# Optimization experiments

Measured on AMD Instinct MI355X. Metric: run time of the kernel, lower is better.

## Reference

```python
import jax, jax.numpy as jnp
import numpy as np

B, T, N, D = 16, 12, 325, 1
K, H = 3, 64
ST, Z, LH = 95, 32, 128
MI = ST + Z  # 127


def _mlp(x, w1, b1, w2, b2):
    return jnp.maximum(x @ w1 + b1, 0.0) @ w2 + b2


def setup_inputs() -> dict:
    key = jax.random.key(0)
    ks = jax.random.split(key, 20)
    inp = {
        "G": jax.random.normal(ks[0], (K, N, N), jnp.float32) * (1.0 / np.sqrt(N)),
        "x": jax.random.normal(ks[1], (B, T, N, D), jnp.float32),
        "meta_input": jax.random.normal(ks[2], (B, N, MI), jnp.float32),
    }
    s = 0.02
    outs = {"lwg": K * (D + H) * 2 * H, "lbg": 2 * H, "lwu": K * (D + H) * H, "lbu": H}
    i = 3
    for name, od in outs.items():
        inp[name + "_w1"] = jax.random.normal(ks[i], (MI, LH), jnp.float32) * s; i += 1
        inp[name + "_b1"] = jnp.zeros((LH,), jnp.float32)
        inp[name + "_w2"] = jax.random.normal(ks[i], (LH, od), jnp.float32) * s; i += 1
        inp[name + "_b2"] = jnp.zeros((od,), jnp.float32)
    return inp


def reference(G, x, meta_input,
              lwg_w1, lwg_b1, lwg_w2, lwg_b2,
              lbg_w1, lbg_b1, lbg_w2, lbg_b2,
              lwu_w1, lwu_b1, lwu_w2, lwu_b2,
              lbu_w1, lbu_b1, lbu_w2, lbu_b2):
    # hypernetwork: per-(batch, node) GCN weights
    Wg = _mlp(meta_input, lwg_w1, lwg_b1, lwg_w2, lwg_b2).reshape(B, N, K * (D + H), 2 * H)
    bg = _mlp(meta_input, lbg_w1, lbg_b1, lbg_w2, lbg_b2)          # [B,N,2H]
    Wu = _mlp(meta_input, lwu_w1, lwu_b1, lwu_w2, lwu_b2).reshape(B, N, K * (D + H), H)
    bu = _mlp(meta_input, lbu_w1, lbu_b1, lbu_w2, lbu_b2)          # [B,N,H]

    def gcn(inp, W, b):
        # Chebyshev hops stacked along k (matches torch.cat over k-blocks)
        sup = jnp.einsum('knm,bmi->bnki', G, inp)                  # [B,N,K,i]
        sup = sup.reshape(B, N, -1)                                # [B,N,K*i]
        return jnp.einsum('bni,bnih->bnh', sup, W) + b

    def step(h, xt):
        comb = jnp.concatenate([xt, h], axis=-1)                   # [B,N,D+H]
        zr = jax.nn.sigmoid(gcn(comb, Wg, bg))
        z, r = zr[..., :H], zr[..., H:]
        cand = jnp.concatenate([xt, r * h], axis=-1)
        n = jnp.tanh(gcn(cand, Wu, bu))
        h = z * n + (1.0 - z) * h
        return h, h

    h0 = jnp.zeros((B, N, H), x.dtype)
    h_last, hs = jax.lax.scan(step, h0, jnp.moveaxis(x, 1, 0))     # hs: [T,B,N,H]
    return jnp.moveaxis(hs, 0, 1), h_last
```

## Files before the change

kernel.cpp:

```cpp
#include <hip/hip_runtime.h>
#include <hip/hip_bf16.h>
#include <stdint.h>

#define Bc   16
#define Tc   12
#define Nc   325
#define Kc   3
#define Hc   64
#define MIc  127
#define LHc  128
#define BNc  (Bc*Nc)
#define SUPW 195
#define NCg  (SUPW*2*Hc)
#define NCu  (SUPW*Hc)
#define MP   163
#define MCH  6

typedef _Float16 half8  __attribute__((ext_vector_type(8)));
typedef _Float16 half2v __attribute__((ext_vector_type(2)));
typedef float    f32x4  __attribute__((ext_vector_type(4)));

static __device__ __forceinline__ float bflo(unsigned int u) {
    return __uint_as_float(u << 16);
}
static __device__ __forceinline__ float bfhi(unsigned int u) {
    return __uint_as_float(u & 0xffff0000u);
}
static __device__ __forceinline__ unsigned short f2bf(float f) {
    unsigned int u = __float_as_uint(f);
    unsigned int r = (u + 0x7fffu + ((u >> 16) & 1u)) >> 16;
    return (unsigned short)r;
}
static __device__ __forceinline__ float fdot2f(half2v a, half2v b, float c) {
#if defined(__has_builtin)
#if __has_builtin(__builtin_amdgcn_fdot2)
    return __builtin_amdgcn_fdot2(a, b, c, false);
#else
    return c + (float)a[0] * (float)b[0] + (float)a[1] * (float)b[1];
#endif
#else
    return c + (float)a[0] * (float)b[0] + (float)a[1] * (float)b[1];
#endif
}
static __device__ __forceinline__ unsigned int packh2(float a, float b) {
    half2v h; h[0] = (_Float16)a; h[1] = (_Float16)b;
    return *(unsigned int*)&h;
}

__global__ __launch_bounds__(128) void meta1_kernel(
    const float* __restrict__ meta,
    const float* __restrict__ w1a, const float* __restrict__ b1a,
    const float* __restrict__ w1b, const float* __restrict__ b1b,
    const float* __restrict__ w1c, const float* __restrict__ b1c,
    const float* __restrict__ w1d, const float* __restrict__ b1d,
    _Float16* __restrict__ r1a, _Float16* __restrict__ r1b,
    _Float16* __restrict__ r1c, _Float16* __restrict__ r1d)
{
    __shared__ float mrow[4][128];
    const int bn0 = blockIdx.x * 4;
    const int l   = threadIdx.x;
#pragma unroll
    for (int r = 0; r < 4; r++)
        mrow[r][l] = (l < MIc) ? meta[(size_t)(bn0 + r) * MIc + l] : 0.f;
    __syncthreads();

    const float* w1s[4] = {w1a, w1b, w1c, w1d};
    const float* b1s[4] = {b1a, b1b, b1c, b1d};
    _Float16*    os[4]  = {r1a, r1b, r1c, r1d};
#pragma unroll
    for (int s = 0; s < 4; s++) {
        const float* w = w1s[s];
        float acc[4];
        const float bv = b1s[s][l];
#pragma unroll
        for (int r = 0; r < 4; r++) acc[r] = bv;
        for (int m = 0; m < MIc; m++) {
            float wv = w[m * LHc + l];
#pragma unroll
            for (int r = 0; r < 4; r++) acc[r] = fmaf(mrow[r][m], wv, acc[r]);
        }
#pragma unroll
        for (int r = 0; r < 4; r++)
            os[s][(size_t)(bn0 + r) * LHc + l] = (_Float16)fmaxf(acc[r], 0.f);
    }
}

__global__ __launch_bounds__(256) void transpose_w2_kernel(
    const float* __restrict__ w2, _Float16* __restrict__ w2t, int NC)
{
    __shared__ float Ls[128][65];
    const int c0 = blockIdx.x * 64;
    const int t  = threadIdx.x;
    {
        const int c  = t & 63;
        const int kb = t >> 6;
        for (int k = kb; k < 128; k += 4) {
            int cc = c0 + c;
            Ls[k][c] = (cc < NC) ? w2[(size_t)k * NC + cc] : 0.f;
        }
    }
    __syncthreads();
    {
        const int k  = t & 127;
        const int ch = t >> 7;
        for (int c = ch; c < 64; c += 2) {
            int cc = c0 + c;
            if (cc < NC) w2t[(size_t)cc * 128 + k] = (_Float16)Ls[k][c];
        }
    }
}

template<bool BF16OUT>
__global__ __launch_bounds__(256) void meta2_mfma_kernel(
    const _Float16* __restrict__ A,
    const _Float16* __restrict__ Bt,
    const float* __restrict__ bias,
    void* __restrict__ outp, int NC, int nrows)
{
    __shared__ __align__(16) _Float16 As[64][136];
    __shared__ __align__(16) _Float16 Bs[64][136];
    __shared__ unsigned short Cs[64][72];
    const int t  = threadIdx.x;
    const int w  = t >> 6;
    const int l  = t & 63;
    const int r0 = blockIdx.x * 64;
    const int c0 = blockIdx.y * 64;

#pragma unroll
    for (int p = 0; p < 4; p++) {
        const int gid = p * 256 + t;
        const int row = gid >> 4;
        const int cg  = gid & 15;
        half8 av = (half8)(_Float16)0.f;
        if (r0 + row < nrows) av = *(const half8*)(A + (size_t)(r0 + row) * 128 + cg * 8);
        *(half8*)&As[row][cg * 8] = av;
        half8 bv = *(const half8*)(Bt + (size_t)(c0 + row) * 128 + cg * 8);
        *(half8*)&Bs[row][cg * 8] = bv;
    }
    __syncthreads();

    const int lr = l & 15;
    const int lk = l >> 4;

    half8 aF[4];
#pragma unroll
    for (int kk = 0; kk < 4; kk++)
        aF[kk] = *(const half8*)&As[w * 16 + lr][kk * 32 + lk * 8];

    f32x4 acc[4];
#pragma unroll
    for (int j = 0; j < 4; j++) acc[j] = (f32x4)0.f;

#pragma unroll
    for (int j = 0; j < 4; j++)
#pragma unroll
        for (int kk = 0; kk < 4; kk++) {
            half8 bF = *(const half8*)&Bs[j * 16 + lr][kk * 32 + lk * 8];
            acc[j] = __builtin_amdgcn_mfma_f32_16x16x32_f16(aF[kk], bF, acc[j], 0, 0, 0);
        }

    if (BF16OUT) {
#pragma unroll
        for (int j = 0; j < 4; j++) {
            const float bv = bias[c0 + j * 16 + lr];
#pragma unroll
            for (int q = 0; q < 4; q++)
                Cs[w * 16 + lk * 4 + q][j * 16 + lr] = f2bf(acc[j][q] + bv);
        }
        __syncthreads();
        const int rl  = t >> 2;
        const int cp  = t & 3;
        const int row = r0 + rl;
        if (row < nrows) {
            const uint4* src = (const uint4*)&Cs[rl][cp * 16];
            uint4* dst = (uint4*)((unsigned short*)outp + (size_t)row * NC + c0 + cp * 16);
            dst[0] = src[0];
            dst[1] = src[1];
        }
    } else {
#pragma unroll
        for (int j = 0; j < 4; j++) {
            const int col = c0 + j * 16 + lr;
            const float bv = bias[col];
#pragma unroll
            for (int q = 0; q < 4; q++) {
                const int row = r0 + w * 16 + lk * 4 + q;
                if (row < nrows)
                    ((float*)outp)[(size_t)row * NC + col] = acc[j][q] + bv;
            }
        }
    }
}

__global__ __launch_bounds__(256) void gx_kernel(
    const float* __restrict__ G, const float* __restrict__ x,
    float* __restrict__ GX)
{
    __shared__ __align__(16) float Gs[32][36];
    __shared__ __align__(16) float Xs[32][65];
    const int k   = blockIdx.x;
    const int n0  = blockIdx.y * 32;
    const int tb0 = blockIdx.z * 64;
    const int t   = threadIdx.x;
    const int j   = t & 63;
    const int ng  = t >> 6;

    float acc[8] = {0.f,0.f,0.f,0.f,0.f,0.f,0.f,0.f};

    for (int mc = 0; mc < 11; mc++) {
        const int m0 = mc * 32;
        __syncthreads();
        {
            const int ln  = t >> 3;
            const int lm0 = (t & 7) * 4;
            const int gn  = n0 + ln;
#pragma unroll
            for (int u = 0; u < 4; u++) {
                int m = m0 + lm0 + u;
                Gs[lm0 + u][ln] = (gn < Nc && m < Nc) ? G[((size_t)k * Nc + gn) * Nc + m] : 0.f;
            }
        }
        {
            const int row = t >> 2;
            const int ms  = (t & 3) * 8;
            const float* xr = x + (size_t)(tb0 + row) * Nc;
#pragma unroll
            for (int u = 0; u < 8; u++) {
                int m = m0 + ms + u;
                Xs[ms + u][row] = (m < Nc) ? xr[m] : 0.f;
            }
        }
        __syncthreads();
#pragma unroll
        for (int mm = 0; mm < 32; mm++) {
            float xv = Xs[mm][j];
            float4 ga = *(const float4*)&Gs[mm][ng * 8];
            float4 gb = *(const float4*)&Gs[mm][ng * 8 + 4];
            acc[0] = fmaf(ga.x, xv, acc[0]);
            acc[1] = fmaf(ga.y, xv, acc[1]);
            acc[2] = fmaf(ga.z, xv, acc[2]);
            acc[3] = fmaf(ga.w, xv, acc[3]);
            acc[4] = fmaf(gb.x, xv, acc[4]);
            acc[5] = fmaf(gb.y, xv, acc[5]);
            acc[6] = fmaf(gb.z, xv, acc[6]);
            acc[7] = fmaf(gb.w, xv, acc[7]);
        }
    }

    const int tb = tb0 + j;
    const int b  = tb / Tc;
    const int tv = tb % Tc;
    float* gxp = GX + (((size_t)tv * Bc + b) * Kc + k) * Nc;
#pragma unroll
    for (int i = 0; i < 8; i++) {
        int n = n0 + ng * 8 + i;
        if (n < Nc) gxp[n] = acc[i];
    }
}

__global__ __launch_bounds__(256, 6) void fused_gates_kernel(
    const float* __restrict__ G, const float* __restrict__ hbuf,
    const float* __restrict__ GX, const unsigned short* __restrict__ Wg,
    const float* __restrict__ bg, float* __restrict__ zbuf,
    float* __restrict__ rhbuf, int tt, int bStart)
{
    __shared__ unsigned int Hc2[32][64];
    __shared__ unsigned int Gc2[3][34];
    __shared__ float supL[208];
    __shared__ float pS[4][16][8];
    const int bx = blockIdx.x;
    const int bl = bx / Nc;
    const int n  = bx % Nc;
    const int b  = bStart + bl;
    const int t  = threadIdx.x;
    const int lane = t & 63;
    const int w  = t >> 6;
    const int j  = lane;

    const float* hb = hbuf + (size_t)b * Nc * Hc;
    float accA = 0.f;

    for (int c6 = 0; c6 < MCH; c6++) {
        const int mpB = c6 * 32;
        __syncthreads();
#pragma unroll
        for (int p = 0; p < 8; p++) {
            const int idx = p * 256 + t;
            const int mpl = idx >> 6;
            const int jj  = idx & 63;
            const int m0  = 2 * (mpB + mpl);
            float h0 = (m0 < Nc)     ? hb[(size_t)m0 * Hc + jj]       : 0.f;
            float h1 = (m0 + 1 < Nc) ? hb[(size_t)(m0 + 1) * Hc + jj] : 0.f;
            Hc2[mpl][jj] = packh2(h0, h1);
        }
        if (t < 96) {
            const int kk  = t >> 5;
            const int mpl = t & 31;
            const int m0  = 2 * (mpB + mpl);
            const float* gr = G + ((size_t)kk * Nc + n) * Nc;
            float g0 = (m0 < Nc)     ? gr[m0]     : 0.f;
            float g1 = (m0 + 1 < Nc) ? gr[m0 + 1] : 0.f;
            Gc2[kk][mpl] = packh2(g0, g1);
        }
        __syncthreads();
        if (w < 3) {
            const unsigned int* gp = &Gc2[w][0];
#pragma unroll
            for (int mpl = 0; mpl < 32; mpl++) {
                unsigned int hu = Hc2[mpl][j];
                unsigned int gu = gp[mpl];
                accA = fdot2f(*(half2v*)&gu, *(half2v*)&hu, accA);
            }
        }
    }
    if (w < 3) supL[w * 65 + 1 + j] = accA;
    if (t < 3)
        supL[t * 65] = GX[(((size_t)tt * Bc + b) * Kc + t) * Nc + n];
    __syncthreads();

    const int c = lane & 15;
    const int g = lane >> 4;
    const unsigned short* wrow = Wg + ((size_t)bl * Nc + n) * NCg;
    float a2[8] = {0.f,0.f,0.f,0.f,0.f,0.f,0.f,0.f};

#pragma unroll
    for (int i0 = 0; i0 < SUPW; i0 += 16) {
        const int i = i0 + w * 4 + g;
        if (i < SUPW) {
            uint4 v = *(const uint4*)(wrow + (size_t)i * 128 + c * 8);
            float s = supL[i];
            a2[0] = fmaf(s, bflo(v.x), a2[0]);
            a2[1] = fmaf(s, bfhi(v.x), a2[1]);
            a2[2] = fmaf(s, bflo(v.y), a2[2]);
            a2[3] = fmaf(s, bfhi(v.y), a2[3]);
            a2[4] = fmaf(s, bflo(v.z), a2[4]);
            a2[5] = fmaf(s, bfhi(v.z), a2[5]);
            a2[6] = fmaf(s, bflo(v.w), a2[6]);
            a2[7] = fmaf(s, bfhi(v.w), a2[7]);
        }
    }
#pragma unroll
    for (int e = 0; e < 8; e++) {
        a2[e] += __shfl_xor(a2[e], 16, 64);
        a2[e] += __shfl_xor(a2[e], 32, 64);
    }
    if (g == 0) {
#pragma unroll
        for (int e = 0; e < 8; e++) pS[w][c][e] = a2[e];
    }
    __syncthreads();
    if (w == 0 && g == 0) {
        const size_t bng = (size_t)b * Nc + n;
#pragma unroll
        for (int e = 0; e < 8; e++) {
            const int h2 = c * 8 + e;
            const float pre = pS[0][c][e] + pS[1][c][e] + pS[2][c][e] + pS[3][c][e]
                            + bg[bng * (2 * Hc) + h2];
            const float zr  = 1.f / (1.f + expf(-pre));
            if (h2 < Hc) zbuf[bng * Hc + h2] = zr;
            else {
                const int hh = h2 - Hc;
                rhbuf[bng * Hc + hh] = zr * hbuf[bng * Hc + hh];
            }
        }
    }
}

__global__ __launch_bounds__(256, 6) void fused_update_kernel(
    const float* __restrict__ G, const float* __restrict__ rhbuf,
    const float* __restrict__ GX, const unsigned short* __restrict__ Wu,
    const float* __restrict__ bu, const float* __restrict__ zbuf,
    float* __restrict__ hbuf, float* __restrict__ outp, int tt, int bStart)
{
    __shared__ unsigned int Hc2[32][64];
    __shared__ unsigned int Gc2[3][34];
    __shared__ float supL[208];
    __shared__ float pS[4][8][8];
    const int bx = blockIdx.x;
    const int bl = bx / Nc;
    const int n  = bx % Nc;
    const int b  = bStart + bl;
    const int t  = threadIdx.x;
    const int lane = t & 63;
    const int w  = t >> 6;
    const int j  = lane;

    const float* hb = rhbuf + (size_t)b * Nc * Hc;
    float accA = 0.f;

    for (int c6 = 0; c6 < MCH; c6++) {
        const int mpB = c6 * 32;
        __syncthreads();
#pragma unroll
        for (int p = 0; p < 8; p++) {
            const int idx = p * 256 + t;
            const int mpl = idx >> 6;
            const int jj  = idx & 63;
            const int m0  = 2 * (mpB + mpl);
            float h0 = (m0 < Nc)     ? hb[(size_t)m0 * Hc + jj]       : 0.f;
            float h1 = (m0 + 1 < Nc) ? hb[(size_t)(m0 + 1) * Hc + jj] : 0.f;
            Hc2[mpl][jj] = packh2(h0, h1);
        }
        if (t < 96) {
            const int kk  = t >> 5;
            const int mpl = t & 31;
            const int m0  = 2 * (mpB + mpl);
            const float* gr = G + ((size_t)kk * Nc + n) * Nc;
            float g0 = (m0 < Nc)     ? gr[m0]     : 0.f;
            float g1 = (m0 + 1 < Nc) ? gr[m0 + 1] : 0.f;
            Gc2[kk][mpl] = packh2(g0, g1);
        }
        __syncthreads();
        if (w < 3) {
            const unsigned int* gp = &Gc2[w][0];
#pragma unroll
            for (int mpl = 0; mpl < 32; mpl++) {
                unsigned int hu = Hc2[mpl][j];
                unsigned int gu = gp[mpl];
                accA = fdot2f(*(half2v*)&gu, *(half2v*)&hu, accA);
            }
        }
    }
    if (w < 3) supL[w * 65 + 1 + j] = accA;
    if (t < 3)
        supL[t * 65] = GX[(((size_t)tt * Bc + b) * Kc + t) * Nc + n];
    __syncthreads();

    const int c = lane & 7;
    const int g = lane >> 3;
    const unsigned short* wrow = Wu + ((size_t)bl * Nc + n) * NCu;
    float a2[8] = {0.f,0.f,0.f,0.f,0.f,0.f,0.f,0.f};

#pragma unroll
    for (int i0 = 0; i0 < SUPW; i0 += 32) {
        const int i = i0 + w * 8 + g;
        if (i < SUPW) {
            uint4 v = *(const uint4*)(wrow + (size_t)i * 64 + c * 8);
            float s = supL[i];
            a2[0] = fmaf(s, bflo(v.x), a2[0]);
            a2[1] = fmaf(s, bfhi(v.x), a2[1]);
            a2[2] = fmaf(s, bflo(v.y), a2[2]);
            a2[3] = fmaf(s, bfhi(v.y), a2[3]);
            a2[4] = fmaf(s, bflo(v.z), a2[4]);
            a2[5] = fmaf(s, bfhi(v.z), a2[5]);
            a2[6] = fmaf(s, bflo(v.w), a2[6]);
            a2[7] = fmaf(s, bfhi(v.w), a2[7]);
        }
    }
#pragma unroll
    for (int e = 0; e < 8; e++) {
        a2[e] += __shfl_xor(a2[e], 8, 64);
        a2[e] += __shfl_xor(a2[e], 16, 64);
        a2[e] += __shfl_xor(a2[e], 32, 64);
    }
    if (g == 0) {
#pragma unroll
        for (int e = 0; e < 8; e++) pS[w][c][e] = a2[e];
    }
    __syncthreads();
    if (w == 0 && g == 0) {
        const size_t bng = (size_t)b * Nc + n;
#pragma unroll
        for (int e = 0; e < 8; e++) {
            const int hh = c * 8 + e;
            const float npre = pS[0][c][e] + pS[1][c][e] + pS[2][c][e] + pS[3][c][e]
                             + bu[bng * Hc + hh];
            const float nn_t = tanhf(npre);
            const float z    = zbuf[bng * Hc + hh];
            const float hold = hbuf[bng * Hc + hh];
            const float hnew = fmaf(z, nn_t - hold, hold);
            hbuf[bng * Hc + hh] = hnew;
            outp[(((size_t)b * Tc + tt) * Nc + n) * Hc + hh] = hnew;
            if (tt == Tc - 1)
                outp[(size_t)Bc * Tc * Nc * Hc + bng * Hc + hh] = hnew;
        }
    }
}

extern "C" void kernel_launch(void* const* d_in, const int* in_sizes, int n_in,
                              void* d_out, int out_size, void* d_ws, size_t ws_size,
                              hipStream_t stream)
{
    const float* G        = (const float*)d_in[0];
    const float* x        = (const float*)d_in[1];
    const float* meta     = (const float*)d_in[2];
    const float* lwg_w1   = (const float*)d_in[3];
    const float* lwg_b1   = (const float*)d_in[4];
    const float* lwg_w2   = (const float*)d_in[5];
    const float* lwg_b2   = (const float*)d_in[6];
    const float* lbg_w1   = (const float*)d_in[7];
    const float* lbg_b1   = (const float*)d_in[8];
    const float* lbg_w2   = (const float*)d_in[9];
    const float* lbg_b2   = (const float*)d_in[10];
    const float* lwu_w1   = (const float*)d_in[11];
    const float* lwu_b1   = (const float*)d_in[12];
    const float* lwu_w2   = (const float*)d_in[13];
    const float* lwu_b2   = (const float*)d_in[14];
    const float* lbu_w1   = (const float*)d_in[15];
    const float* lbu_b1   = (const float*)d_in[16];
    const float* lbu_w2   = (const float*)d_in[17];
    const float* lbu_b2   = (const float*)d_in[18];

    auto alignup = [](size_t b) { return (b + 255) & ~(size_t)255; };
    const size_t miscBytes =
        alignup((size_t)BNc * 2 * Hc * 4) +
        alignup((size_t)BNc * Hc * 4) +
        4 * alignup((size_t)BNc * LHc * 2) +
        alignup((size_t)NCg * 128 * 2) +
        alignup((size_t)NCu * 128 * 2) +
        alignup((size_t)128 * 128 * 2) +
        alignup((size_t)64 * 128 * 2) +
        alignup((size_t)Tc * Bc * Kc * Nc * 4) +
        3 * alignup((size_t)BNc * Hc * 4);

    int Bch = 0;
    const int cand[4] = {8, 4, 2, 1};
    for (int ci = 0; ci < 4; ci++) {
        size_t BNch = (size_t)cand[ci] * Nc;
        size_t need = miscBytes + alignup(BNch * NCg * 2) + alignup(BNch * NCu * 2);
        if (need <= ws_size) { Bch = cand[ci]; break; }
    }
    if (Bch == 0) return;
    const int nChunks = Bc / Bch;
    const int BNch    = Bch * Nc;

    char* ws = (char*)d_ws;
    size_t off = 0;
    auto alloc = [&](size_t bytes) -> char* {
        char* p = ws + off;
        off += (bytes + 255) & ~(size_t)255;
        return p;
    };
    unsigned short* Wg = (unsigned short*)alloc((size_t)BNch * NCg * 2);
    unsigned short* Wu = (unsigned short*)alloc((size_t)BNch * NCu * 2);
    float* bgbuf  = (float*)alloc((size_t)BNc * 2 * Hc * 4);
    float* bubuf  = (float*)alloc((size_t)BNc * Hc * 4);
    _Float16* r1g  = (_Float16*)alloc((size_t)BNc * LHc * 2);
    _Float16* r1bg = (_Float16*)alloc((size_t)BNc * LHc * 2);
    _Float16* r1u  = (_Float16*)alloc((size_t)BNc * LHc * 2);
    _Float16* r1bu = (_Float16*)alloc((size_t)BNc * LHc * 2);
    _Float16* w2tg  = (_Float16*)alloc((size_t)NCg * 128 * 2);
    _Float16* w2tu  = (_Float16*)alloc((size_t)NCu * 128 * 2);
    _Float16* w2tbg = (_Float16*)alloc((size_t)128 * 128 * 2);
    _Float16* w2tbu = (_Float16*)alloc((size_t)64 * 128 * 2);
    float* GX    = (float*)alloc((size_t)Tc * Bc * Kc * Nc * 4);
    float* hbuf  = (float*)alloc((size_t)BNc * Hc * 4);
    float* zbuf  = (float*)alloc((size_t)BNc * Hc * 4);
    float* rhbuf = (float*)alloc((size_t)BNc * Hc * 4);
    if (off > ws_size) return;

    float* out = (float*)d_out;

    hipMemsetAsync(hbuf, 0, (size_t)BNc * Hc * 4, stream);

    meta1_kernel<<<BNc / 4, 128, 0, stream>>>(
        meta, lwg_w1, lwg_b1, lbg_w1, lbg_b1, lwu_w1, lwu_b1, lbu_w1, lbu_b1,
        r1g, r1bg, r1u, r1bu);

    transpose_w2_kernel<<<(NCg + 63) / 64, 256, 0, stream>>>(lwg_w2, w2tg, NCg);
    transpose_w2_kernel<<<(NCu + 63) / 64, 256, 0, stream>>>(lwu_w2, w2tu, NCu);
    transpose_w2_kernel<<<2, 256, 0, stream>>>(lbg_w2, w2tbg, 2 * Hc);
    transpose_w2_kernel<<<1, 256, 0, stream>>>(lbu_w2, w2tbu, Hc);

    meta2_mfma_kernel<false><<<dim3((BNc + 63) / 64, (2 * Hc) / 64), 256, 0, stream>>>(
        r1bg, w2tbg, lbg_b2, (void*)bgbuf, 2 * Hc, BNc);
    meta2_mfma_kernel<false><<<dim3((BNc + 63) / 64, Hc / 64), 256, 0, stream>>>(
        r1bu, w2tbu, lbu_b2, (void*)bubuf, Hc, BNc);

    gx_kernel<<<dim3(Kc, 11, 3), 256, 0, stream>>>(G, x, GX);

    for (int ch = 0; ch < nChunks; ch++) {
        const int bStart  = ch * Bch;
        const int bnStart = bStart * Nc;

        meta2_mfma_kernel<true><<<dim3((BNch + 63) / 64, NCg / 64), 256, 0, stream>>>(
            r1g + (size_t)bnStart * LHc, w2tg, lwg_b2, (void*)Wg, NCg, BNch);
        meta2_mfma_kernel<true><<<dim3((BNch + 63) / 64, NCu / 64), 256, 0, stream>>>(
            r1u + (size_t)bnStart * LHc, w2tu, lwu_b2, (void*)Wu, NCu, BNch);

        for (int tt = 0; tt < Tc; tt++) {
            fused_gates_kernel<<<Bch * Nc, 256, 0, stream>>>(
                G, hbuf, GX, Wg, bgbuf, zbuf, rhbuf, tt, bStart);
            fused_update_kernel<<<Bch * Nc, 256, 0, stream>>>(
                G, rhbuf, GX, Wu, bubuf, zbuf, hbuf, out, tt, bStart);
        }
    }
}
```

Before: 2.141 ms.

## Prefetch per-node GCN weights into LDS via async global_load_lds during support phase

At kernel start, each block issues asynchronous global-to-LDS loads of its per-node bf16 weight slab (49 KB for gates, 25 KB for update). The hop aggregation over the hidden state then runs while those loads are in flight, and the weight matvec reads from LDS instead of global memory. The weight buffers are padded by 1 KB so the whole-kilobyte copies cannot read past the end. Occupancy hints drop to 2 and 4 blocks per CU because of the larger LDS footprint, which may reduce latency hiding. There is no explicit vmcnt wait before the LDS reads, which relies on the intervening __syncthreads.

After: 3.243 ms. 51.5% more time.

```diff
diff --git a/kernel.cpp b/kernel.cpp
--- a/kernel.cpp
+++ b/kernel.cpp
@@ -15,6 +15,8 @@
 #define NCu  (SUPW*Hc)
 #define MP   163
 #define MCH  6
+#define WGRG 49
+#define WGRU 25
 
 typedef _Float16 half8  __attribute__((ext_vector_type(8)));
 typedef _Float16 half2v __attribute__((ext_vector_type(2)));
@@ -45,6 +47,20 @@
 static __device__ __forceinline__ unsigned int packh2(float a, float b) {
     half2v h; h[0] = (_Float16)a; h[1] = (_Float16)b;
     return *(unsigned int*)&h;
+}
+
+static __device__ __forceinline__ void gload_lds_1k(
+    const char* gsrc, char* ldst, int lane)
+{
+#if defined(__has_builtin) && __has_builtin(__builtin_amdgcn_global_load_lds)
+    __builtin_amdgcn_global_load_lds(
+        (const __attribute__((address_space(1))) unsigned int*)(gsrc + lane * 16),
+        (__attribute__((address_space(3))) unsigned int*)(ldst + lane * 16),
+        16, 0, 0);
+#else
+    uint4 v = *(const uint4*)(gsrc + lane * 16);
+    *(uint4*)(ldst + lane * 16) = v;
+#endif
 }
 
 __global__ __launch_bounds__(128) void meta1_kernel(
@@ -258,12 +274,13 @@
     }
 }
 
-__global__ __launch_bounds__(256, 6) void fused_gates_kernel(
+__global__ __launch_bounds__(256, 2) void fused_gates_kernel(
     const float* __restrict__ G, const float* __restrict__ hbuf,
     const float* __restrict__ GX, const unsigned short* __restrict__ Wg,
     const float* __restrict__ bg, float* __restrict__ zbuf,
     float* __restrict__ rhbuf, int tt, int bStart)
 {
+    __shared__ __align__(16) unsigned short Wld[WGRG * 512];
     __shared__ unsigned int Hc2[32][64];
     __shared__ unsigned int Gc2[3][34];
     __shared__ float supL[208];
@@ -277,6 +294,13 @@
     const int w  = t >> 6;
     const int j  = lane;
 
+    {
+        const char* wsrc = (const char*)(Wg + ((size_t)bl * Nc + n) * NCg);
+        char* ldst = (char*)Wld;
+        for (int q = w; q < WGRG; q += 4)
+            gload_lds_1k(wsrc + q * 1024, ldst + q * 1024, lane);
+    }
+
     const float* hb = hbuf + (size_t)b * Nc * Hc;
     float accA = 0.f;
 
@@ -320,14 +344,13 @@
 
     const int c = lane & 15;
     const int g = lane >> 4;
-    const unsigned short* wrow = Wg + ((size_t)bl * Nc + n) * NCg;
     float a2[8] = {0.f,0.f,0.f,0.f,0.f,0.f,0.f,0.f};
 
 #pragma unroll
     for (int i0 = 0; i0 < SUPW; i0 += 16) {
         const int i = i0 + w * 4 + g;
         if (i < SUPW) {
-            uint4 v = *(const uint4*)(wrow + (size_t)i * 128 + c * 8);
+            uint4 v = *(const uint4*)(Wld + i * 128 + c * 8);
             float s = supL[i];
             a2[0] = fmaf(s, bflo(v.x), a2[0]);
             a2[1] = fmaf(s, bfhi(v.x), a2[1]);
@@ -366,12 +389,13 @@
     }
 }
 
-__global__ __launch_bounds__(256, 6) void fused_update_kernel(
+__global__ __launch_bounds__(256, 4) void fused_update_kernel(
     const float* __restrict__ G, const float* __restrict__ rhbuf,
     const float* __restrict__ GX, const unsigned short* __restrict__ Wu,
     const float* __restrict__ bu, const float* __restrict__ zbuf,
     float* __restrict__ hbuf, float* __restrict__ outp, int tt, int bStart)
 {
+    __shared__ __align__(16) unsigned short Wld[WGRU * 512];
     __shared__ unsigned int Hc2[32][64];
     __shared__ unsigned int Gc2[3][34];
     __shared__ float supL[208];
@@ -385,6 +409,13 @@
     const int w  = t >> 6;
     const int j  = lane;
 
+    {
+        const char* wsrc = (const char*)(Wu + ((size_t)bl * Nc + n) * NCu);
+        char* ldst = (char*)Wld;
+        for (int q = w; q < WGRU; q += 4)
+            gload_lds_1k(wsrc + q * 1024, ldst + q * 1024, lane);
+    }
+
     const float* hb = rhbuf + (size_t)b * Nc * Hc;
     float accA = 0.f;
 
@@ -428,14 +459,13 @@
 
     const int c = lane & 7;
     const int g = lane >> 3;
-    const unsigned short* wrow = Wu + ((size_t)bl * Nc + n) * NCu;
     float a2[8] = {0.f,0.f,0.f,0.f,0.f,0.f,0.f,0.f};
 
 #pragma unroll
     for (int i0 = 0; i0 < SUPW; i0 += 32) {
         const int i = i0 + w * 8 + g;
         if (i < SUPW) {
-            uint4 v = *(const uint4*)(wrow + (size_t)i * 64 + c * 8);
+            uint4 v = *(const uint4*)(Wld + i * 64 + c * 8);
             float s = supL[i];
             a2[0] = fmaf(s, bflo(v.x), a2[0]);
             a2[1] = fmaf(s, bfhi(v.x), a2[1]);
@@ -517,7 +547,8 @@
     const int cand[4] = {8, 4, 2, 1};
     for (int ci = 0; ci < 4; ci++) {
         size_t BNch = (size_t)cand[ci] * Nc;
-        size_t need = miscBytes + alignup(BNch * NCg * 2) + alignup(BNch * NCu * 2);
+        size_t need = miscBytes + alignup(BNch * NCg * 2 + 1024)
+                                + alignup(BNch * NCu * 2 + 1024);
         if (need <= ws_size) { Bch = cand[ci]; break; }
     }
     if (Bch == 0) return;
@@ -531,8 +562,8 @@
         off += (bytes + 255) & ~(size_t)255;
         return p;
     };
-    unsigned short* Wg = (unsigned short*)alloc((size_t)BNch * NCg * 2);
-    unsigned short* Wu = (unsigned short*)alloc((size_t)BNch * NCu * 2);
+    unsigned short* Wg = (unsigned short*)alloc((size_t)BNch * NCg * 2 + 1024);
+    unsigned short* Wu = (unsigned short*)alloc((size_t)BNch * NCu * 2 + 1024);
     float* bgbuf  = (float*)alloc((size_t)BNc * 2 * Hc * 4);
     float* bubuf  = (float*)alloc((size_t)BNc * Hc * 4);
     _Float16* r1g  = (_Float16*)alloc((size_t)BNc * LHc * 2);
```

## Store gate hypernetwork weights in scaled FP8 and prestage full G rows

Applied to the files above, without the earlier changes.

The generated gate weights Wg are now written as FP8 e4m3 with a fixed scale of 16, not bf16. The gates kernel decodes them with the hardware fp8 convert and multiplies the result by the inverse scale. This halves the bytes streamed per timestep for the largest weight tensor, and the smaller footprint may allow bigger batch chunks. Both recurrent kernels also stage all three G rows into shared memory once up front instead of reloading a slice in every chunk. The cost is much coarser weight precision, which risks accuracy failures, plus extra shared memory.

Result: faster. 1.902 ms (median of 2 runs) (-11.2%).

```diff
diff --git a/kernel.cpp b/kernel.cpp
--- a/kernel.cpp
+++ b/kernel.cpp
@@ -1,5 +1,6 @@
 #include <hip/hip_runtime.h>
 #include <hip/hip_bf16.h>
+#include <hip/hip_fp8.h>
 #include <stdint.h>
 
 #define Bc   16
@@ -15,6 +16,9 @@
 #define NCu  (SUPW*Hc)
 #define MP   163
 #define MCH  6
+#define GTW  192
+#define WSCL 16.0f
+#define WINV 0.0625f
 
 typedef _Float16 half8  __attribute__((ext_vector_type(8)));
 typedef _Float16 half2v __attribute__((ext_vector_type(2)));
@@ -46,6 +50,19 @@
     half2v h; h[0] = (_Float16)a; h[1] = (_Float16)b;
     return *(unsigned int*)&h;
 }
+static __device__ __forceinline__ unsigned char f2fp8(float f) {
+    __hip_fp8_e4m3 t(f);
+    return t.__x;
+}
+#if defined(__has_builtin) && __has_builtin(__builtin_amdgcn_cvt_f32_fp8)
+#define FP8TOF(wrd, sel) __builtin_amdgcn_cvt_f32_fp8((wrd), (sel))
+#else
+static __device__ __forceinline__ float fp8tof_sw(unsigned int wrd, int sel) {
+    __hip_fp8_e4m3 t; t.__x = (unsigned char)(wrd >> (sel * 8));
+    return (float)t;
+}
+#define FP8TOF(wrd, sel) fp8tof_sw((wrd), (sel))
+#endif
 
 __global__ __launch_bounds__(128) void meta1_kernel(
     const float* __restrict__ meta,
@@ -110,7 +127,7 @@
     }
 }
 
-template<bool BF16OUT>
+template<int OM>
 __global__ __launch_bounds__(256) void meta2_mfma_kernel(
     const _Float16* __restrict__ A,
     const _Float16* __restrict__ Bt,
@@ -119,7 +136,8 @@
 {
     __shared__ __align__(16) _Float16 As[64][136];
     __shared__ __align__(16) _Float16 Bs[64][136];
-    __shared__ unsigned short Cs[64][72];
+    __shared__ __align__(16) unsigned short Cs[64][72];
+    __shared__ __align__(16) unsigned char  Cs8[64][80];
     const int t  = threadIdx.x;
     const int w  = t >> 6;
     const int l  = t & 63;
@@ -159,7 +177,7 @@
             acc[j] = __builtin_amdgcn_mfma_f32_16x16x32_f16(aF[kk], bF, acc[j], 0, 0, 0);
         }
 
-    if (BF16OUT) {
+    if (OM == 1) {
 #pragma unroll
         for (int j = 0; j < 4; j++) {
             const float bv = bias[c0 + j * 16 + lr];
@@ -176,6 +194,24 @@
             uint4* dst = (uint4*)((unsigned short*)outp + (size_t)row * NC + c0 + cp * 16);
             dst[0] = src[0];
             dst[1] = src[1];
+        }
+    } else if (OM == 2) {
+#pragma unroll
+        for (int j = 0; j < 4; j++) {
+            const float bv = bias[c0 + j * 16 + lr];
+#pragma unroll
+            for (int q = 0; q < 4; q++)
+                Cs8[w * 16 + lk * 4 + q][j * 16 + lr] =
+                    f2fp8((acc[j][q] + bv) * WSCL);
+        }
+        __syncthreads();
+        const int rl  = t >> 2;
+        const int cp  = t & 3;
+        const int row = r0 + rl;
+        if (row < nrows) {
+            const uint4* src = (const uint4*)&Cs8[rl][cp * 16];
+            uint4* dst = (uint4*)((unsigned char*)outp + (size_t)row * NC + c0 + cp * 16);
+            dst[0] = src[0];
         }
     } else {
 #pragma unroll
@@ -258,14 +294,141 @@
     }
 }
 
+static __device__ __forceinline__ void stage_g_rows(
+    const float* __restrict__ G, int n, unsigned int (&Gt)[3][GTW])
+{
+    const int t = threadIdx.x;
+    for (int idx = t; idx < 3 * GTW; idx += 256) {
+        const int kk = idx / GTW;
+        const int mp = idx % GTW;
+        const float* gr = G + ((size_t)kk * Nc + n) * Nc;
+        const int m0 = 2 * mp;
+        float g0 = (m0 < Nc)     ? gr[m0]     : 0.f;
+        float g1 = (m0 + 1 < Nc) ? gr[m0 + 1] : 0.f;
+        Gt[kk][mp] = packh2(g0, g1);
+    }
+}
+
 __global__ __launch_bounds__(256, 6) void fused_gates_kernel(
     const float* __restrict__ G, const float* __restrict__ hbuf,
-    const float* __restrict__ GX, const unsigned short* __restrict__ Wg,
+    const float* __restrict__ GX, const unsigned char* __restrict__ Wg,
     const float* __restrict__ bg, float* __restrict__ zbuf,
     float* __restrict__ rhbuf, int tt, int bStart)
 {
     __shared__ unsigned int Hc2[32][64];
-    __shared__ unsigned int Gc2[3][34];
+    __shared__ unsigned int Gt1[3][GTW];
+    __shared__ float supL[208];
+    __shared__ float pS[4][8][16];
+    const int bx = blockIdx.x;
+    const int bl = bx / Nc;
+    const int n  = bx % Nc;
+    const int b  = bStart + bl;
+    const int t  = threadIdx.x;
+    const int lane = t & 63;
+    const int w  = t >> 6;
+    const int j  = lane;
+
+    stage_g_rows(G, n, Gt1);
+
+    const float* hb = hbuf + (size_t)b * Nc * Hc;
+    float accA = 0.f;
+
+    for (int c6 = 0; c6 < MCH; c6++) {
+        const int mpB = c6 * 32;
+        __syncthreads();
+#pragma unroll
+        for (int p = 0; p < 8; p++) {
+            const int idx = p * 256 + t;
+            const int mpl = idx >> 6;
+            const int jj  = idx & 63;
+            const int m0  = 2 * (mpB + mpl);
+            float h0 = (m0 < Nc)     ? hb[(size_t)m0 * Hc + jj]       : 0.f;
+            float h1 = (m0 + 1 < Nc) ? hb[(size_t)(m0 + 1) * Hc + jj] : 0.f;
+            Hc2[mpl][jj] = packh2(h0, h1);
+        }
+        __syncthreads();
+        if (w < 3) {
+            const unsigned int* gp = &Gt1[w][mpB];
+#pragma unroll
+            for (int mpl = 0; mpl < 32; mpl++) {
+                unsigned int hu = Hc2[mpl][j];
+                unsigned int gu = gp[mpl];
+                accA = fdot2f(*(half2v*)&gu, *(half2v*)&hu, accA);
+            }
+        }
+    }
+    if (w < 3) supL[w * 65 + 1 + j] = accA;
+    if (t < 3)
+        supL[t * 65] = GX[(((size_t)tt * Bc + b) * Kc + t) * Nc + n];
+    __syncthreads();
+
+    const int c = lane & 7;
+    const int g = lane >> 3;
+    const unsigned char* wrow = Wg + ((size_t)bl * Nc + n) * NCg;
+    float a2[16];
+#pragma unroll
+    for (int e = 0; e < 16; e++) a2[e] = 0.f;
+
+#pragma unroll
+    for (int i0 = 0; i0 < SUPW; i0 += 32) {
+        const int i = i0 + w * 8 + g;
+        if (i < SUPW) {
+            uint4 v = *(const uint4*)(wrow + (size_t)i * 128 + c * 16);
+            float s = supL[i];
+            a2[0]  = fmaf(s, FP8TOF(v.x, 0), a2[0]);
+            a2[1]  = fmaf(s, FP8TOF(v.x, 1), a2[1]);
+            a2[2]  = fmaf(s, FP8TOF(v.x, 2), a2[2]);
+            a2[3]  = fmaf(s, FP8TOF(v.x, 3), a2[3]);
+            a2[4]  = fmaf(s, FP8TOF(v.y, 0), a2[4]);
+            a2[5]  = fmaf(s, FP8TOF(v.y, 1), a2[5]);
+            a2[6]  = fmaf(s, FP8TOF(v.y, 2), a2[6]);
+            a2[7]  = fmaf(s, FP8TOF(v.y, 3), a2[7]);
+            a2[8]  = fmaf(s, FP8TOF(v.z, 0), a2[8]);
+            a2[9]  = fmaf(s, FP8TOF(v.z, 1), a2[9]);
+            a2[10] = fmaf(s, FP8TOF(v.z, 2), a2[10]);
+            a2[11] = fmaf(s, FP8TOF(v.z, 3), a2[11]);
+            a2[12] = fmaf(s, FP8TOF(v.w, 0), a2[12]);
+            a2[13] = fmaf(s, FP8TOF(v.w, 1), a2[13]);
+            a2[14] = fmaf(s, FP8TOF(v.w, 2), a2[14]);
+            a2[15] = fmaf(s, FP8TOF(v.w, 3), a2[15]);
+        }
+    }
+#pragma unroll
+    for (int e = 0; e < 16; e++) {
+        a2[e] += __shfl_xor(a2[e], 8, 64);
+        a2[e] += __shfl_xor(a2[e], 16, 64);
+        a2[e] += __shfl_xor(a2[e], 32, 64);
+    }
+    if (g == 0) {
+#pragma unroll
+        for (int e = 0; e < 16; e++) pS[w][c][e] = a2[e];
+    }
+    __syncthreads();
+    if (w == 0 && g == 0) {
+        const size_t bng = (size_t)b * Nc + n;
+#pragma unroll
+        for (int e = 0; e < 16; e++) {
+            const int h2 = c * 16 + e;
+            const float pre = (pS[0][c][e] + pS[1][c][e] + pS[2][c][e] + pS[3][c][e]) * WINV
+                            + bg[bng * (2 * Hc) + h2];
+            const float zr  = 1.f / (1.f + expf(-pre));
+            if (h2 < Hc) zbuf[bng * Hc + h2] = zr;
+            else {
+                const int hh = h2 - Hc;
+                rhbuf[bng * Hc + hh] = zr * hbuf[bng * Hc + hh];
+            }
+        }
+    }
+}
+
+__global__ __launch_bounds__(256, 6) void fused_update_kernel(
+    const float* __restrict__ G, const float* __restrict__ rhbuf,
+    const float* __restrict__ GX, const unsigned short* __restrict__ Wu,
+    const float* __restrict__ bu, const float* __restrict__ zbuf,
+    float* __restrict__ hbuf, float* __restrict__ outp, int tt, int bStart)
+{
+    __shared__ unsigned int Hc2[32][64];
+    __shared__ unsigned int Gt1[3][GTW];
     __shared__ float supL[208];
     __shared__ float pS[4][16][8];
     const int bx = blockIdx.x;
@@ -277,7 +440,9 @@
     const int w  = t >> 6;
     const int j  = lane;
 
-    const float* hb = hbuf + (size_t)b * Nc * Hc;
+    stage_g_rows(G, n, Gt1);
+
+    const float* hb = rhbuf + (size_t)b * Nc * Hc;
     float accA = 0.f;
 
     for (int c6 = 0; c6 < MCH; c6++) {
@@ -293,126 +458,9 @@
             float h1 = (m0 + 1 < Nc) ? hb[(size_t)(m0 + 1) * Hc + jj] : 0.f;
             Hc2[mpl][jj] = packh2(h0, h1);
         }
-        if (t < 96) {
-            const int kk  = t >> 5;
-            const int mpl = t & 31;
-            const int m0  = 2 * (mpB + mpl);
-            const float* gr = G + ((size_t)kk * Nc + n) * Nc;
-            float g0 = (m0 < Nc)     ? gr[m0]     : 0.f;
-            float g1 = (m0 + 1 < Nc) ? gr[m0 + 1] : 0.f;
-            Gc2[kk][mpl] = packh2(g0, g1);
-        }
         __syncthreads();
         if (w < 3) {
-            const unsigned int* gp = &Gc2[w][0];
-#pragma unroll
-            for (int mpl = 0; mpl < 32; mpl++) {
-                unsigned int hu = Hc2[mpl][j];
-                unsigned int gu = gp[mpl];
-                accA = fdot2f(*(half2v*)&gu, *(half2v*)&hu, accA);
-            }
-        }
-    }
-    if (w < 3) supL[w * 65 + 1 + j] = accA;
-    if (t < 3)
-        supL[t * 65] = GX[(((size_t)tt * Bc + b) * Kc + t) * Nc + n];
-    __syncthreads();
-
-    const int c = lane & 15;
-    const int g = lane >> 4;
-    const unsigned short* wrow = Wg + ((size_t)bl * Nc + n) * NCg;
-    float a2[8] = {0.f,0.f,0.f,0.f,0.f,0.f,0.f,0.f};
-
-#pragma unroll
-    for (int i0 = 0; i0 < SUPW; i0 += 16) {
-        const int i = i0 + w * 4 + g;
-        if (i < SUPW) {
-            uint4 v = *(const uint4*)(wrow + (size_t)i * 128 + c * 8);
-            float s = supL[i];
-            a2[0] = fmaf(s, bflo(v.x), a2[0]);
-            a2[1] = fmaf(s, bfhi(v.x), a2[1]);
-            a2[2] = fmaf(s, bflo(v.y), a2[2]);
-            a2[3] = fmaf(s, bfhi(v.y), a2[3]);
-            a2[4] = fmaf(s, bflo(v.z), a2[4]);
-            a2[5] = fmaf(s, bfhi(v.z), a2[5]);
-            a2[6] = fmaf(s, bflo(v.w), a2[6]);
-            a2[7] = fmaf(s, bfhi(v.w), a2[7]);
-        }
-    }
-#pragma unroll
-    for (int e = 0; e < 8; e++) {
-        a2[e] += __shfl_xor(a2[e], 16, 64);
-        a2[e] += __shfl_xor(a2[e], 32, 64);
-    }
-    if (g == 0) {
-#pragma unroll
-        for (int e = 0; e < 8; e++) pS[w][c][e] = a2[e];
-    }
-    __syncthreads();
-    if (w == 0 && g == 0) {
-        const size_t bng = (size_t)b * Nc + n;
-#pragma unroll
-        for (int e = 0; e < 8; e++) {
-            const int h2 = c * 8 + e;
-            const float pre = pS[0][c][e] + pS[1][c][e] + pS[2][c][e] + pS[3][c][e]
-                            + bg[bng * (2 * Hc) + h2];
-            const float zr  = 1.f / (1.f + expf(-pre));
-            if (h2 < Hc) zbuf[bng * Hc + h2] = zr;
-            else {
-                const int hh = h2 - Hc;
-                rhbuf[bng * Hc + hh] = zr * hbuf[bng * Hc + hh];
-            }
-        }
-    }
-}
-
-__global__ __launch_bounds__(256, 6) void fused_update_kernel(
-    const float* __restrict__ G, const float* __restrict__ rhbuf,
-    const float* __restrict__ GX, const unsigned short* __restrict__ Wu,
-    const float* __restrict__ bu, const float* __restrict__ zbuf,
-    float* __restrict__ hbuf, float* __restrict__ outp, int tt, int bStart)
-{
-    __shared__ unsigned int Hc2[32][64];
-    __shared__ unsigned int Gc2[3][34];
-    __shared__ float supL[208];
-    __shared__ float pS[4][8][8];
-    const int bx = blockIdx.x;
-    const int bl = bx / Nc;
-    const int n  = bx % Nc;
-    const int b  = bStart + bl;
-    const int t  = threadIdx.x;
-    const int lane = t & 63;
-    const int w  = t >> 6;
-    const int j  = lane;
-
-    const float* hb = rhbuf + (size_t)b * Nc * Hc;
-    float accA = 0.f;
-
-    for (int c6 = 0; c6 < MCH; c6++) {
-        const int mpB = c6 * 32;
-        __syncthreads();
-#pragma unroll
-        for (int p = 0; p < 8; p++) {
-            const int idx = p * 256 + t;
-            const int mpl = idx >> 6;
-            const int jj  = idx & 63;
-            const int m0  = 2 * (mpB + mpl);
-            float h0 = (m0 < Nc)     ? hb[(size_t)m0 * Hc + jj]       : 0.f;
-            float h1 = (m0 + 1 < Nc) ? hb[(size_t)(m0 + 1) * Hc + jj] : 0.f;
-            Hc2[mpl][jj] = packh2(h0, h1);
-        }
-        if (t < 96) {
-            const int kk  = t >> 5;
-            const int mpl = t & 31;
-            const int m0  = 2 * (mpB + mpl);
-            const float* gr = G + ((size_t)kk * Nc + n) * Nc;
-            float g0 = (m0 < Nc)     ? gr[m0]     : 0.f;
-            float g1 = (m0 + 1 < Nc) ? gr[m0 + 1] : 0.f;
-            Gc2[kk][mpl] = packh2(g0, g1);
-        }
-        __syncthreads();
-        if (w < 3) {
-            const unsigned int* gp = &Gc2[w][0];
+            const unsigned int* gp = &Gt1[w][mpB];
 #pragma unroll
             for (int mpl = 0; mpl < 32; mpl++) {
                 unsigned int hu = Hc2[mpl][j];
@@ -517,7 +565,7 @@
     const int cand[4] = {8, 4, 2, 1};
     for (int ci = 0; ci < 4; ci++) {
         size_t BNch = (size_t)cand[ci] * Nc;
-        size_t need = miscBytes + alignup(BNch * NCg * 2) + alignup(BNch * NCu * 2);
+        size_t need = miscBytes + alignup(BNch * NCg) + alignup(BNch * NCu * 2);
         if (need <= ws_size) { Bch = cand[ci]; break; }
     }
     if (Bch == 0) return;
@@ -531,7 +579,7 @@
         off += (bytes + 255) & ~(size_t)255;
         return p;
     };
-    unsigned short* Wg = (unsigned short*)alloc((size_t)BNch * NCg * 2);
+    unsigned char*  Wg = (unsigned char*)alloc((size_t)BNch * NCg);
     unsigned short* Wu = (unsigned short*)alloc((size_t)BNch * NCu * 2);
     float* bgbuf  = (float*)alloc((size_t)BNc * 2 * Hc * 4);
     float* bubuf  = (float*)alloc((size_t)BNc * Hc * 4);
@@ -562,9 +610,9 @@
     transpose_w2_kernel<<<2, 256, 0, stream>>>(lbg_w2, w2tbg, 2 * Hc);
     transpose_w2_kernel<<<1, 256, 0, stream>>>(lbu_w2, w2tbu, Hc);
 
-    meta2_mfma_kernel<false><<<dim3((BNc + 63) / 64, (2 * Hc) / 64), 256, 0, stream>>>(
+    meta2_mfma_kernel<0><<<dim3((BNc + 63) / 64, (2 * Hc) / 64), 256, 0, stream>>>(
         r1bg, w2tbg, lbg_b2, (void*)bgbuf, 2 * Hc, BNc);
-    meta2_mfma_kernel<false><<<dim3((BNc + 63) / 64, Hc / 64), 256, 0, stream>>>(
+    meta2_mfma_kernel<0><<<dim3((BNc + 63) / 64, Hc / 64), 256, 0, stream>>>(
         r1bu, w2tbu, lbu_b2, (void*)bubuf, Hc, BNc);
 
     gx_kernel<<<dim3(Kc, 11, 3), 256, 0, stream>>>(G, x, GX);
@@ -573,15 +621,15 @@
         const int bStart  = ch * Bch;
         const int bnStart = bStart * Nc;
 
-        meta2_mfma_kernel<true><<<dim3((BNch + 63) / 64, NCg / 64), 256, 0, stream>>>(
+        meta2_mfma_kernel<2><<<dim3((BNch + 63) / 64, NCg / 64), 256, 0, stream>>>(
             r1g + (size_t)bnStart * LHc, w2tg, lwg_b2, (void*)Wg, NCg, BNch);
-        meta2_mfma_kernel<true><<<dim3((BNch + 63) / 64, NCu / 64), 256, 0, stream>>>(
+        meta2_mfma_kernel<1><<<dim3((BNch + 63) / 64, NCu / 64), 256, 0, stream>>>(
             r1u + (size_t)bnStart * LHc, w2tu, lwu_b2, (void*)Wu, NCu, BNch);
 
         for (int tt = 0; tt < Tc; tt++) {
-            fused_gates_kernel<<<Bch * Nc, 256, 0, stream>>>(
+            fused_gates_kernel<<<BNch, 256, 0, stream>>>(
                 G, hbuf, GX, Wg, bgbuf, zbuf, rhbuf, tt, bStart);
-            fused_update_kernel<<<Bch * Nc, 256, 0, stream>>>(
+            fused_update_kernel<<<BNch, 256, 0, stream>>>(
                 G, rhbuf, GX, Wu, bubuf, zbuf, hbuf, out, tt, bStart);
         }
     }
```
